# Kernel tuning notes

Hardware: AMD Instinct MI355X
Metric: run time of the kernel (lower is better)

## Reference

```python
import jax, jax.numpy as jnp
import numpy as np

N_NODES = 50000
N_EDGES = 1600000
NUM_GRAPHS = 64


def gcn_conv(x, edge_index, edge_weight, W, b):
    # PyG GCNConv with normalize=False: h = x @ W; out[i] = sum_{e: tgt(e)=i} w_e * h[src(e)]; out += b
    h = x @ W                                   # [N, out]
    src, tgt = edge_index[0], edge_index[1]
    msg = h[src] * edge_weight[:, None]         # [E, out] gather + scale
    out = jax.ops.segment_sum(msg, tgt, num_segments=N_NODES)
    return out + b


def setup_inputs() -> dict:
    key = jax.random.key(0)
    ks = jax.random.split(key, 10)
    x = jax.random.normal(ks[0], (N_NODES, 128), dtype=jnp.float32)
    edge_index = jax.random.randint(ks[1], (2, N_EDGES), 0, N_NODES, dtype=jnp.int64)
    edge_weight = jax.random.uniform(ks[2], (N_EDGES,), dtype=jnp.float32)
    batch = jnp.sort(jax.random.randint(ks[3], (N_NODES,), 0, NUM_GRAPHS, dtype=jnp.int64))
    W1 = jax.random.normal(ks[4], (128, 64), dtype=jnp.float32) * 0.09  # ~glorot scale
    b1 = jax.random.normal(ks[5], (64,), dtype=jnp.float32) * 0.01
    W2 = jax.random.normal(ks[6], (64, 64), dtype=jnp.float32) * 0.125
    b2 = jax.random.normal(ks[7], (64,), dtype=jnp.float32) * 0.01
    W3 = jax.random.normal(ks[8], (64, 64), dtype=jnp.float32) * 0.125
    b3 = jax.random.normal(ks[9], (64,), dtype=jnp.float32) * 0.01
    return {"x": x, "edge_index": edge_index, "edge_weight": edge_weight, "batch": batch,
            "W1": W1, "b1": b1, "W2": W2, "b2": b2, "W3": W3, "b3": b3}


def reference(x, edge_index, edge_weight, batch, W1, b1, W2, b2, W3, b3):
    # dropout is identity in eval mode
    h = jax.nn.relu(gcn_conv(x, edge_index, edge_weight, W1, b1))
    embed = gcn_conv(h, edge_index, edge_weight, W2, b2)
    graph = gcn_conv(h, edge_index, edge_weight, W3, b3)
    graph_embed = jax.ops.segment_sum(graph, batch, num_segments=NUM_GRAPHS)
    return (embed, graph_embed)
```

## Files before the change

kernel.cpp:

```cpp
#include <hip/hip_runtime.h>


typedef _Float16 f16;
typedef _Float16 h2v __attribute__((ext_vector_type(2)));
typedef _Float16 h4v __attribute__((ext_vector_type(4)));

#define THREADS 256
#define BTHREADS 1024
#define NODECAP 80
#define NC 391
#define CSTRIDE 16
#define ACH 4096
#define CAPC 4736

#define SMEM_BYTES (128 * 68 * 2)

__device__ __forceinline__ void bin_coarse_body(
    int bid, char* smem, const int* __restrict__ src,
    const int* __restrict__ tgt, const float* __restrict__ ew,
    int* __restrict__ cnt_a, int2* __restrict__ cbins, int E) {
  int* lcnt  = (int*)smem;
  int* gbase = lcnt + NC;
  int tid = threadIdx.x;
  for (int i = tid; i < NC; i += THREADS) lcnt[i] = 0;
  __syncthreads();

  int e0 = bid * ACH;
  int xr[16], wr[16], cr[16];
#pragma unroll
  for (int k = 0; k < 16; ++k) {
    int e = e0 + k * THREADS + tid;
    if (e < E) {
      int t = tgt[e];
      int c = t >> 7;
      int r = atomicAdd(&lcnt[c], 1);
      xr[k] = (src[e] & 0xffff) | ((t & 127) << 16);
      wr[k] = __float_as_int(ew[e]);
      cr[k] = c | (r << 16);
    } else {
      cr[k] = -1;
    }
  }
  __syncthreads();

  for (int c = tid; c < NC; c += THREADS) {
    int n = lcnt[c];
    gbase[c] = n ? atomicAdd(&cnt_a[c * CSTRIDE], n) : 0;
  }
  __syncthreads();

#pragma unroll
  for (int k = 0; k < 16; ++k) {
    if (cr[k] < 0) continue;
    int c = cr[k] & 0xffff;
    int r = cr[k] >> 16;
    int dst = gbase[c] + r;
    if (dst < CAPC) cbins[(size_t)c * CAPC + dst] = make_int2(xr[k], wr[k]);
  }
}

__device__ __forceinline__ void gemm1_body(
    int bid, char* smem, const float* __restrict__ A,
    const float* __restrict__ W, f16* __restrict__ C, int M) {
  f16 (*Xs)[68] = (f16(*)[68])smem;
  int tid = threadIdx.x;
  int r0 = bid * 64;

  for (int i = tid * 4; i < 64 * 128; i += THREADS * 4) {
    int row = i >> 7, k = i & 127;
    float4 v = make_float4(0.f, 0.f, 0.f, 0.f);
    if (r0 + row < M) v = *(const float4*)(A + (size_t)(r0 + row) * 128 + k);
    Xs[k + 0][row] = (f16)v.x; Xs[k + 1][row] = (f16)v.y;
    Xs[k + 2][row] = (f16)v.z; Xs[k + 3][row] = (f16)v.w;
  }
  __syncthreads();

  int tx = tid & 15, ty = tid >> 4;
  const float* wp = W + tx * 4;
  float acc[4][4] = {};
#pragma unroll 8
  for (int k = 0; k < 128; ++k) {
    float4 w4 = *(const float4*)(wp + k * 64);
    h4v x4 = *(const h4v*)&Xs[k][ty * 4];
    float xx = (float)x4.x, xy = (float)x4.y, xz = (float)x4.z, xw = (float)x4.w;
    acc[0][0] = fmaf(xx, w4.x, acc[0][0]); acc[0][1] = fmaf(xx, w4.y, acc[0][1]);
    acc[0][2] = fmaf(xx, w4.z, acc[0][2]); acc[0][3] = fmaf(xx, w4.w, acc[0][3]);
    acc[1][0] = fmaf(xy, w4.x, acc[1][0]); acc[1][1] = fmaf(xy, w4.y, acc[1][1]);
    acc[1][2] = fmaf(xy, w4.z, acc[1][2]); acc[1][3] = fmaf(xy, w4.w, acc[1][3]);
    acc[2][0] = fmaf(xz, w4.x, acc[2][0]); acc[2][1] = fmaf(xz, w4.y, acc[2][1]);
    acc[2][2] = fmaf(xz, w4.z, acc[2][2]); acc[2][3] = fmaf(xz, w4.w, acc[2][3]);
    acc[3][0] = fmaf(xw, w4.x, acc[3][0]); acc[3][1] = fmaf(xw, w4.y, acc[3][1]);
    acc[3][2] = fmaf(xw, w4.z, acc[3][2]); acc[3][3] = fmaf(xw, w4.w, acc[3][3]);
  }
#pragma unroll
  for (int i = 0; i < 4; ++i) {
    int r = r0 + ty * 4 + i;
    if (r >= M) continue;
    union { f16 h4[4]; uint2 u; } pk;
    pk.h4[0] = (f16)acc[i][0]; pk.h4[1] = (f16)acc[i][1];
    pk.h4[2] = (f16)acc[i][2]; pk.h4[3] = (f16)acc[i][3];
    *(uint2*)(C + (size_t)r * 64 + tx * 4) = pk.u;
  }
}

__global__ __launch_bounds__(THREADS, 8) void k_bin_gemm(
    const int* __restrict__ src, const int* __restrict__ tgt,
    const float* __restrict__ ew, int* __restrict__ cnt_a,
    int2* __restrict__ cbins, int E,
    const float* __restrict__ x, const float* __restrict__ W1,
    f16* __restrict__ hpre, int M, int NBIN, int NGEMM) {
  __shared__ __align__(16) char smem[SMEM_BYTES];
  int b = blockIdx.x;
  int binid = (b % 3 == 0) ? b / 3 : -1;
  if (binid >= 0 && binid < NBIN) {
    bin_coarse_body(binid, smem, src, tgt, ew, cnt_a, cbins, E);
  } else {
    int nb = min((b + 2) / 3, NBIN);
    int gi = b - nb;
    if (gi < NGEMM) gemm1_body(gi, smem, x, W1, hpre, M);
  }
}

__global__ __launch_bounds__(BTHREADS) void bin_fine(
    const int* __restrict__ cnt_a, const int2* __restrict__ cbins,
    int* __restrict__ cnt_f, int2* __restrict__ fbins, int N) {
  __shared__ int fcnt[128];
  int c = blockIdx.x;
  int tid = threadIdx.x;
  if (tid < 128) fcnt[tid] = 0;
  __syncthreads();
  int d = min(cnt_a[c * CSTRIDE], CAPC);
  const int2* ep = cbins + (size_t)c * CAPC;
  for (int i = tid; i < d; i += BTHREADS) {
    int2 ent = ep[i];
    int tl = ent.x >> 16;
    int r = atomicAdd(&fcnt[tl], 1);
    int node = c * 128 + tl;
    if (r < NODECAP && node < N)
      fbins[(size_t)node * NODECAP + r] = make_int2((ent.x & 0xffff) << 7, ent.y);
  }
  __syncthreads();
  if (tid < 128) {
    int node = c * 128 + tid;
    if (node < N) cnt_f[node] = min(fcnt[tid], NODECAP);
  }
}

template <bool RELU>
__global__ __launch_bounds__(THREADS) void gather_nodes(
    const f16* __restrict__ h, const int2* __restrict__ fbins,
    const int* __restrict__ cnt, const float* __restrict__ bias,
    f16* __restrict__ out, int N) {
  int tid = threadIdx.x;
  int lane = tid & 63;
  int node = blockIdx.x * 4 + (tid >> 6);
  if (node >= N) return;
  int d = min(cnt[node], NODECAP);
  const int2* ep = fbins + (size_t)node * NODECAP;
  const char* hb = (const char*)h;
  int q = lane >> 4;
  int lq = lane & 15;
  int lq8 = lq * 8;
  float4 acc = make_float4(0.f, 0.f, 0.f, 0.f);

  for (int base = 0; base < d; base += 64) {
    int take = min(64, d - base);
    int2 ent = ep[base + min(lane, take - 1)];
    int pv = ent.x;
    float wv = (lane < take) ? __int_as_float(ent.y) : 0.f;

    for (int g0 = 0; g0 < take; g0 += 32) {
      int off[8]; float w[8];
#pragma unroll
      for (int u = 0; u < 8; ++u) {
        int sl = g0 + u * 4 + q;
        off[u] = __shfl(pv, sl, 64);
        w[u]   = __shfl(wv, sl, 64);
      }
      uint2 r8[8];
#pragma unroll
      for (int u = 0; u < 8; ++u)
        r8[u] = *(const uint2*)(hb + off[u] + lq8);
#pragma unroll
      for (int u = 0; u < 8; ++u) {
        h2v p0 = __builtin_bit_cast(h2v, r8[u].x);
        h2v p1 = __builtin_bit_cast(h2v, r8[u].y);
        acc.x = fmaf((float)p0.x, w[u], acc.x);
        acc.y = fmaf((float)p0.y, w[u], acc.y);
        acc.z = fmaf((float)p1.x, w[u], acc.z);
        acc.w = fmaf((float)p1.y, w[u], acc.w);
      }
    }
  }

  acc.x += __shfl_xor(acc.x, 16, 64); acc.x += __shfl_xor(acc.x, 32, 64);
  acc.y += __shfl_xor(acc.y, 16, 64); acc.y += __shfl_xor(acc.y, 32, 64);
  acc.z += __shfl_xor(acc.z, 16, 64); acc.z += __shfl_xor(acc.z, 32, 64);
  acc.w += __shfl_xor(acc.w, 16, 64); acc.w += __shfl_xor(acc.w, 32, 64);

  if (q == 0) {
    union { f16 h4[4]; uint2 u; } pk;
    if (RELU) {
      float4 bb = *(const float4*)(bias + lq * 4);
      pk.h4[0] = (f16)fmaxf(acc.x + bb.x, 0.f);
      pk.h4[1] = (f16)fmaxf(acc.y + bb.y, 0.f);
      pk.h4[2] = (f16)fmaxf(acc.z + bb.z, 0.f);
      pk.h4[3] = (f16)fmaxf(acc.w + bb.w, 0.f);
    } else {
      pk.h4[0] = (f16)acc.x; pk.h4[1] = (f16)acc.y;
      pk.h4[2] = (f16)acc.z; pk.h4[3] = (f16)acc.w;
    }
    *(uint2*)((char*)out + (size_t)node * 128 + lq8) = pk.u;
  }
}

__global__ __launch_bounds__(THREADS) void k_gemm2_reduce(
    const f16* __restrict__ A, const float* __restrict__ W,
    const float* __restrict__ bias, const int* __restrict__ batch,
    float* __restrict__ C, float* __restrict__ B, float* __restrict__ counts,
    int M) {
  __shared__ float Xs[64][68];
  __shared__ float Ws[64][64];
  __shared__ int bsh[64];
  int tid = threadIdx.x;
  int r0 = blockIdx.x * 64;

  for (int i = tid * 4; i < 64 * 64; i += THREADS * 4)
    *(float4*)&Ws[0][i] = *(const float4*)(W + i);
  if (tid < 64) bsh[tid] = (r0 + tid < M) ? batch[r0 + tid] : -1;

  for (int i = tid * 4; i < 64 * 64; i += THREADS * 4) {
    int row = i >> 6, k = i & 63;
    float4 v = make_float4(0.f, 0.f, 0.f, 0.f);
    if (r0 + row < M) {
      uint2 u = *(const uint2*)(A + (size_t)(r0 + row) * 64 + k);
      h2v a0 = __builtin_bit_cast(h2v, u.x);
      h2v a1 = __builtin_bit_cast(h2v, u.y);
      v = make_float4((float)a0.x, (float)a0.y, (float)a1.x, (float)a1.y);
    }
    Xs[k + 0][row] = v.x; Xs[k + 1][row] = v.y;
    Xs[k + 2][row] = v.z; Xs[k + 3][row] = v.w;
  }
  __syncthreads();

  int tx = tid & 15, ty = tid >> 4;
  float acc[4][4] = {};
#pragma unroll 8
  for (int k = 0; k < 64; ++k) {
    float4 w4 = *(const float4*)&Ws[k][tx * 4];
    float4 x4 = *(const float4*)&Xs[k][ty * 4];
    acc[0][0] = fmaf(x4.x, w4.x, acc[0][0]); acc[0][1] = fmaf(x4.x, w4.y, acc[0][1]);
    acc[0][2] = fmaf(x4.x, w4.z, acc[0][2]); acc[0][3] = fmaf(x4.x, w4.w, acc[0][3]);
    acc[1][0] = fmaf(x4.y, w4.x, acc[1][0]); acc[1][1] = fmaf(x4.y, w4.y, acc[1][1]);
    acc[1][2] = fmaf(x4.y, w4.z, acc[1][2]); acc[1][3] = fmaf(x4.y, w4.w, acc[1][3]);
    acc[2][0] = fmaf(x4.z, w4.x, acc[2][0]); acc[2][1] = fmaf(x4.z, w4.y, acc[2][1]);
    acc[2][2] = fmaf(x4.z, w4.z, acc[2][2]); acc[2][3] = fmaf(x4.z, w4.w, acc[2][3]);
    acc[3][0] = fmaf(x4.w, w4.x, acc[3][0]); acc[3][1] = fmaf(x4.w, w4.y, acc[3][1]);
    acc[3][2] = fmaf(x4.w, w4.z, acc[3][2]); acc[3][3] = fmaf(x4.w, w4.w, acc[3][3]);
  }
#pragma unroll
  for (int i = 0; i < 4; ++i) {
    int r = r0 + ty * 4 + i;
    if (r >= M) continue;
    float4 bb = *(const float4*)(bias + tx * 4);
    float4 o = make_float4(acc[i][0] + bb.x, acc[i][1] + bb.y,
                           acc[i][2] + bb.z, acc[i][3] + bb.w);
    *(float4*)(C + (size_t)r * 64 + tx * 4) = o;
  }

  int k = tid & 63, p = tid >> 6;
  float racc = 0.f, rcnt = 0.f;
  int cur = -1;
#pragma unroll 4
  for (int j = 0; j < 16; ++j) {
    int row = p * 16 + j;
    if (r0 + row >= M) break;
    int g = bsh[row];
    if (g != cur) {
      if (cur >= 0) {
        unsafeAtomicAdd(&B[cur * 64 + k], racc);
        if (k == 0) unsafeAtomicAdd(&counts[cur], rcnt);
      }
      racc = 0.f; rcnt = 0.f; cur = g;
    }
    racc += Xs[k][row];
    rcnt += 1.f;
  }
  if (cur >= 0) {
    unsafeAtomicAdd(&B[cur * 64 + k], racc);
    if (k == 0) unsafeAtomicAdd(&counts[cur], rcnt);
  }
}

__global__ __launch_bounds__(THREADS) void graph_out_k(
    const float* __restrict__ B, const float* __restrict__ W3,
    const float* __restrict__ b3, const float* __restrict__ counts,
    float* __restrict__ out, int G) {
  int j = threadIdx.x & 63;
  int g = blockIdx.x * (THREADS >> 6) + (threadIdx.x >> 6);
  if (g >= G) return;
  float acc = 0.f;
#pragma unroll
  for (int k = 0; k < 64; ++k) acc += B[g * 64 + k] * W3[k * 64 + j];
  out[g * 64 + j] = acc + counts[g] * b3[j];
}

extern "C" void kernel_launch(void* const* d_in, const int* in_sizes, int n_in,
                              void* d_out, int out_size, void* d_ws, size_t ws_size,
                              hipStream_t stream) {
  const float* x     = (const float*)d_in[0];
  const int*   ei    = (const int*)d_in[1];
  const float* ew    = (const float*)d_in[2];
  const int*   batch = (const int*)d_in[3];
  const float* W1    = (const float*)d_in[4];
  const float* b1    = (const float*)d_in[5];
  const float* W2    = (const float*)d_in[6];
  const float* b2    = (const float*)d_in[7];
  const float* W3    = (const float*)d_in[8];
  const float* b3    = (const float*)d_in[9];

  const int N = in_sizes[0] / 128;
  const int E = in_sizes[1] / 2;
  const int G = (out_size - N * 64) / 64;
  const int* src = ei;
  const int* tgt = ei + E;
  const int NBIN = (E + ACH - 1) / ACH;
  const int NGEMM = (N + 63) / 64;

  float* out_embed = (float*)d_out;
  float* out_graph = (float*)d_out + (size_t)N * 64;

  char* ws = (char*)d_ws;
  f16*   hpre   = (f16*)ws;
  f16*   h1     = hpre + (size_t)N * 64;
  f16*   A      = h1 + (size_t)N * 64;
  int*   cnt_f  = (int*)(A + (size_t)N * 64);
  int*   cnt_a  = cnt_f + N;
  float* B      = (float*)(cnt_a + NC * CSTRIDE);
  float* counts = B + (size_t)G * 64;
  size_t zero_bytes = (size_t)NC * CSTRIDE * 4 + (size_t)(G * 64 + G) * 4;
  size_t off = ((size_t)((char*)(counts + G) - ws) + 255) & ~(size_t)255;
  int2*  fbins  = (int2*)(ws + off);
  off += (size_t)N * NODECAP * 8;
  off = (off + 255) & ~(size_t)255;
  int2*  cbins  = (int2*)(ws + off);

  hipMemsetAsync(cnt_a, 0, zero_bytes, stream);

  k_bin_gemm<<<NBIN + NGEMM, THREADS, 0, stream>>>(
      src, tgt, ew, cnt_a, cbins, E, x, W1, hpre, N, NBIN, NGEMM);

  bin_fine<<<NC, BTHREADS, 0, stream>>>(cnt_a, cbins, cnt_f, fbins, N);

  const int gblocks = (N + 3) / 4;
  gather_nodes<true><<<gblocks, THREADS, 0, stream>>>(
      hpre, fbins, cnt_f, b1, h1, N);
  gather_nodes<false><<<gblocks, THREADS, 0, stream>>>(
      h1, fbins, cnt_f, nullptr, A, N);

  k_gemm2_reduce<<<NGEMM, THREADS, 0, stream>>>(
      A, W2, b2, batch, out_embed, B, counts, N);

  graph_out_k<<<(G + 3) / 4, THREADS, 0, stream>>>(B, W3, b3, counts, out_graph, G);
}
```

Measured before the change: 233.1 us.

## Bin edges directly into per-node buckets with global atomics, dropping coarse stage

Replaces the two-stage binning with a single direct scatter. The old path used LDS-counted coarse bins, a staging buffer and a separate fine-bin kernel. Each edge now takes a slot with a global atomicAdd on its target node's counter and writes straight into that node's bucket. This removes one kernel launch and the write-then-read round trip through the coarse bin buffer. In exchange it issues one global atomic per edge on randomly spread node counters, which costs more than shared-memory atomics, and the per-node counter array must now be zeroed.

New measurement: 299.4 us. 28.4% more time.

```diff
diff --git a/kernel.cpp b/kernel.cpp
--- a/kernel.cpp
+++ b/kernel.cpp
@@ -6,57 +6,38 @@
 typedef _Float16 h4v __attribute__((ext_vector_type(4)));
 
 #define THREADS 256
-#define BTHREADS 1024
 #define NODECAP 80
-#define NC 391
-#define CSTRIDE 16
 #define ACH 4096
-#define CAPC 4736
+#define NBINB(E) (((E) + ACH - 1) / ACH)
 
 #define SMEM_BYTES (128 * 68 * 2)
 
-__device__ __forceinline__ void bin_coarse_body(
-    int bid, char* smem, const int* __restrict__ src,
-    const int* __restrict__ tgt, const float* __restrict__ ew,
-    int* __restrict__ cnt_a, int2* __restrict__ cbins, int E) {
-  int* lcnt  = (int*)smem;
-  int* gbase = lcnt + NC;
+__device__ __forceinline__ void bin_direct_body(
+    int bid, const int* __restrict__ src, const int* __restrict__ tgt,
+    const float* __restrict__ ew, int* __restrict__ cnt_f,
+    int2* __restrict__ fbins, int E) {
   int tid = threadIdx.x;
-  for (int i = tid; i < NC; i += THREADS) lcnt[i] = 0;
-  __syncthreads();
-
   int e0 = bid * ACH;
-  int xr[16], wr[16], cr[16];
+  int t[16], sx[16], wv[16];
+  bool v[16];
 #pragma unroll
   for (int k = 0; k < 16; ++k) {
     int e = e0 + k * THREADS + tid;
-    if (e < E) {
-      int t = tgt[e];
-      int c = t >> 7;
-      int r = atomicAdd(&lcnt[c], 1);
-      xr[k] = (src[e] & 0xffff) | ((t & 127) << 16);
-      wr[k] = __float_as_int(ew[e]);
-      cr[k] = c | (r << 16);
-    } else {
-      cr[k] = -1;
-    }
-  }
-  __syncthreads();
-
-  for (int c = tid; c < NC; c += THREADS) {
-    int n = lcnt[c];
-    gbase[c] = n ? atomicAdd(&cnt_a[c * CSTRIDE], n) : 0;
-  }
-  __syncthreads();
-
-#pragma unroll
-  for (int k = 0; k < 16; ++k) {
-    if (cr[k] < 0) continue;
-    int c = cr[k] & 0xffff;
-    int r = cr[k] >> 16;
-    int dst = gbase[c] + r;
-    if (dst < CAPC) cbins[(size_t)c * CAPC + dst] = make_int2(xr[k], wr[k]);
-  }
+    v[k] = e < E;
+    if (v[k]) {
+      t[k]  = tgt[e];
+      sx[k] = src[e] << 7;
+      wv[k] = __float_as_int(ew[e]);
+    }
+  }
+  int r[16];
+#pragma unroll
+  for (int k = 0; k < 16; ++k)
+    if (v[k]) r[k] = atomicAdd(&cnt_f[t[k]], 1);
+#pragma unroll
+  for (int k = 0; k < 16; ++k)
+    if (v[k] && r[k] < NODECAP)
+      fbins[(size_t)t[k] * NODECAP + r[k]] = make_int2(sx[k], wv[k]);
 }
 
 __device__ __forceinline__ void gemm1_body(
@@ -105,44 +86,19 @@
 
 __global__ __launch_bounds__(THREADS, 8) void k_bin_gemm(
     const int* __restrict__ src, const int* __restrict__ tgt,
-    const float* __restrict__ ew, int* __restrict__ cnt_a,
-    int2* __restrict__ cbins, int E,
+    const float* __restrict__ ew, int* __restrict__ cnt_f,
+    int2* __restrict__ fbins, int E,
     const float* __restrict__ x, const float* __restrict__ W1,
     f16* __restrict__ hpre, int M, int NBIN, int NGEMM) {
   __shared__ __align__(16) char smem[SMEM_BYTES];
   int b = blockIdx.x;
   int binid = (b % 3 == 0) ? b / 3 : -1;
   if (binid >= 0 && binid < NBIN) {
-    bin_coarse_body(binid, smem, src, tgt, ew, cnt_a, cbins, E);
+    bin_direct_body(binid, src, tgt, ew, cnt_f, fbins, E);
   } else {
     int nb = min((b + 2) / 3, NBIN);
     int gi = b - nb;
     if (gi < NGEMM) gemm1_body(gi, smem, x, W1, hpre, M);
-  }
-}
-
-__global__ __launch_bounds__(BTHREADS) void bin_fine(
-    const int* __restrict__ cnt_a, const int2* __restrict__ cbins,
-    int* __restrict__ cnt_f, int2* __restrict__ fbins, int N) {
-  __shared__ int fcnt[128];
-  int c = blockIdx.x;
-  int tid = threadIdx.x;
-  if (tid < 128) fcnt[tid] = 0;
-  __syncthreads();
-  int d = min(cnt_a[c * CSTRIDE], CAPC);
-  const int2* ep = cbins + (size_t)c * CAPC;
-  for (int i = tid; i < d; i += BTHREADS) {
-    int2 ent = ep[i];
-    int tl = ent.x >> 16;
-    int r = atomicAdd(&fcnt[tl], 1);
-    int node = c * 128 + tl;
-    if (r < NODECAP && node < N)
-      fbins[(size_t)node * NODECAP + r] = make_int2((ent.x & 0xffff) << 7, ent.y);
-  }
-  __syncthreads();
-  if (tid < 128) {
-    int node = c * 128 + tid;
-    if (node < N) cnt_f[node] = min(fcnt[tid], NODECAP);
   }
 }
 
@@ -324,7 +280,7 @@
   const int G = (out_size - N * 64) / 64;
   const int* src = ei;
   const int* tgt = ei + E;
-  const int NBIN = (E + ACH - 1) / ACH;
+  const int NBIN = NBINB(E);
   const int NGEMM = (N + 63) / 64;
 
   float* out_embed = (float*)d_out;
@@ -335,22 +291,16 @@
   f16*   h1     = hpre + (size_t)N * 64;
   f16*   A      = h1 + (size_t)N * 64;
   int*   cnt_f  = (int*)(A + (size_t)N * 64);
-  int*   cnt_a  = cnt_f + N;
-  float* B      = (float*)(cnt_a + NC * CSTRIDE);
+  float* B      = (float*)(cnt_f + N);
   float* counts = B + (size_t)G * 64;
-  size_t zero_bytes = (size_t)NC * CSTRIDE * 4 + (size_t)(G * 64 + G) * 4;
+  size_t zero_bytes = (size_t)N * 4 + (size_t)(G * 64 + G) * 4;
   size_t off = ((size_t)((char*)(counts + G) - ws) + 255) & ~(size_t)255;
   int2*  fbins  = (int2*)(ws + off);
-  off += (size_t)N * NODECAP * 8;
-  off = (off + 255) & ~(size_t)255;
-  int2*  cbins  = (int2*)(ws + off);
-
-  hipMemsetAsync(cnt_a, 0, zero_bytes, stream);
+
+  hipMemsetAsync(cnt_f, 0, zero_bytes, stream);
 
   k_bin_gemm<<<NBIN + NGEMM, THREADS, 0, stream>>>(
-      src, tgt, ew, cnt_a, cbins, E, x, W1, hpre, N, NBIN, NGEMM);
-
-  bin_fine<<<NC, BTHREADS, 0, stream>>>(cnt_a, cbins, cnt_f, fbins, N);
+      src, tgt, ew, cnt_f, fbins, E, x, W1, hpre, N, NBIN, NGEMM);
 
   const int gblocks = (N + 3) / 4;
   gather_nodes<true><<<gblocks, THREADS, 0, stream>>>(
```
